# Performance work log

Hardware: AMD Instinct MI355X
Metric: run time of the kernel (lower is better)

Reference implementation:

```python
import jax, jax.numpy as jnp
import numpy as np

B, D, H, O = 32, 128, 256, 10


def setup_inputs() -> dict:
    key = jax.random.key(0)
    ks = jax.random.split(key, 8)
    return {
        "t": jax.random.uniform(ks[0], (1,), dtype=jnp.float32),
        "state_batch": jax.random.normal(ks[1], (2 * B, D), dtype=jnp.float32),
        "x0": jax.random.normal(ks[2], (B, D), dtype=jnp.float32),
        "x1": jax.random.normal(ks[3], (B, D), dtype=jnp.float32),
        "W1": jax.random.normal(ks[4], (D, H), dtype=jnp.float32) / np.sqrt(D),
        "b1": jax.random.normal(ks[5], (H,), dtype=jnp.float32) * 0.01,
        "W2": jax.random.normal(ks[6], (H, O), dtype=jnp.float32) / np.sqrt(H),
        "b2": jax.random.normal(ks[7], (O,), dtype=jnp.float32) * 0.01,
    }


def reference(t, state_batch, x0, x1, W1, b1, W2, b2):
    b = x0.shape[0]
    deviation, dev_velocity = state_batch[:b], state_batch[b:]  # [B,D] each
    tt = t[0]
    window = 4.0 * tt * (1.0 - tt)
    # point on the perturbed path
    x = x0 + tt * (x1 - x0) + window * deviation  # [B,D]

    def f_single(xs):  # [D] -> [O]
        return jnp.tanh(xs @ W1 + b1) @ W2 + b2

    def G_single(xs):  # [D] -> [D,D] pullback metric J^T J + eps I
        J = jax.jacrev(f_single)(xs)  # [O,D] (O small -> reverse mode)
        return J.T @ J + 1e-4 * jnp.eye(xs.shape[0], dtype=xs.dtype)

    # dG[b,i,j,k] = d G_ij / d x_k  -- replaces the torch double autograd loop
    dG = jax.vmap(jax.jacfwd(G_single))(x)  # [B,D,D,D]
    dG = dG / (jnp.sqrt(jnp.sum(dG * dG, axis=(1, 2, 3), keepdims=True)) + 1e-6)
    # Christoffel symbols (first kind, up to normalization as in source)
    Gamma = 0.5 * (dG + jnp.transpose(dG, (0, 2, 1, 3)) - jnp.transpose(dG, (0, 3, 1, 2)))
    a = -jnp.einsum('bijk,bj,bk->bi', Gamma, dev_velocity, dev_velocity)
    a = a / (jnp.linalg.norm(dev_velocity, axis=1, keepdims=True) + 1e-6)
    restoration = -0.1 * deviation
    return jnp.concatenate([dev_velocity, a + restoration], axis=0)  # [2B,D]
```

## Files before the change

### kernel.cpp

```cpp
#include <hip/hip_runtime.h>
#include <hip/hip_bf16.h>


#define NB 32

#define OP    0
#define OE    65536
#define OCW   163840
#define OAUN  245760
#define OVN   249856

template<int BF> __device__ __forceinline__ float ld(const void* p, int i) {
  if constexpr (BF) return __bfloat162float(((const __hip_bfloat16*)p)[i]);
  else return ((const float*)p)[i];
}
template<int BF> __device__ __forceinline__ void st(void* p, int i, float v) {
  if constexpr (BF) ((__hip_bfloat16*)p)[i] = __float2bfloat16(v);
  else ((float*)p)[i] = v;
}
__device__ __forceinline__ float b2f(unsigned short u) {
  return __uint_as_float(((unsigned int)u) << 16);
}
template<int BF> __device__ __forceinline__ float4 ld4(const void* p, int i) {
  if constexpr (BF) {
    ushort4 u = *(const ushort4*)((const unsigned short*)p + i);
    return make_float4(b2f(u.x), b2f(u.y), b2f(u.z), b2f(u.w));
  } else {
    return *(const float4*)((const float*)p + i);
  }
}

__device__ __forceinline__ int blocksniff(const void* sb, int* sh) {
  if (threadIdx.x == 0) *sh = 0;
  __syncthreads();
  float v = fabsf(__bfloat162float(((const __hip_bfloat16*)sb)[threadIdx.x & 255]));
  if (!(v < 1000.0f)) atomicOr(sh, 1);
  __syncthreads();
  return (*sh == 0) ? 1 : 0;
}

#define LXS   0
#define LVS   128
#define LW2   256
#define LYS   2816
#define LRED  2832
#define LF1   2880
#define LEL   4416
#define LSW2  7488
#define LCL   10560
#define LCL2  10660
#define LTOT  10760

#define F1ACC(wv, gidx) do { \
    const float* sp_ = &sm[LSW2 + (gidx)*12]; \
    float4 s0_ = *(const float4*)sp_; \
    float4 s1_ = *(const float4*)(sp_+4); \
    float2 s2_ = *(const float2*)(sp_+8); \
    fa[0]+=(wv)*s0_.x; fa[1]+=(wv)*s0_.y; fa[2]+=(wv)*s0_.z; fa[3]+=(wv)*s0_.w; \
    fa[4]+=(wv)*s1_.x; fa[5]+=(wv)*s1_.y; fa[6]+=(wv)*s1_.z; fa[7]+=(wv)*s1_.w; \
    fa[8]+=(wv)*s2_.x; fa[9]+=(wv)*s2_.y; \
  } while (0)

template<int BF>
__device__ void k1_body(const void* tin, const void* sbin, const void* x0in,
                        const void* x1in, const void* W1in, const void* b1in,
                        const void* W2in, float* ws, float* sm) {
  int bid = blockIdx.x, t = threadIdx.x;
  if (bid >= NB) {
    int row = bid - NB;
    float* colh = sm;
    if (t < 128) colh[t] = ld<BF>(W1in, t * 256 + row);
    __syncthreads();
    float pacc = 0.f;
    for (int d = 0; d < 128; d += 4) {
      float4 c4 = *(const float4*)&colh[d];
      pacc += c4.x * ld<BF>(W1in, (d + 0) * 256 + t);
      pacc += c4.y * ld<BF>(W1in, (d + 1) * 256 + t);
      pacc += c4.z * ld<BF>(W1in, (d + 2) * 256 + t);
      pacc += c4.w * ld<BF>(W1in, (d + 3) * 256 + t);
    }
    ws[OP + row * 256 + t] = pacc;
    return;
  }
  int b = bid;
  int w = t >> 6;
  float tt = ld<BF>(tin, 0);
  float window = 4.f * tt * (1.f - tt);
  if (t < 128) {
    float dev = ld<BF>(sbin, b * 128 + t);
    float v   = ld<BF>(sbin, (NB + b) * 128 + t);
    float x0v = ld<BF>(x0in, b * 128 + t);
    float x1v = ld<BF>(x1in, b * 128 + t);
    sm[LXS + t] = x0v + tt * (x1v - x0v) + window * dev;
    sm[LVS + t] = v;
  }
  for (int i = t; i < 2560; i += 256) sm[LW2 + i] = ld<BF>(W2in, i);
  __syncthreads();
  float hacc = ld<BF>(b1in, t), wacc = 0.f;
  for (int d = 0; d < 128; d += 4) {
    float4 xv = *(const float4*)&sm[LXS + d];
    float4 vv = *(const float4*)&sm[LVS + d];
    float w0 = ld<BF>(W1in, (d + 0) * 256 + t);
    float w1 = ld<BF>(W1in, (d + 1) * 256 + t);
    float w2 = ld<BF>(W1in, (d + 2) * 256 + t);
    float w3 = ld<BF>(W1in, (d + 3) * 256 + t);
    hacc += w0 * xv.x + w1 * xv.y + w2 * xv.z + w3 * xv.w;
    wacc += w0 * vv.x + w1 * vv.y + w2 * vv.z + w3 * vv.w;
  }
  float z  = tanhf(hacc);
  float sg = 1.f - z * z;
  float ug = -2.f * z * sg;
  float w2r[10];
  #pragma unroll
  for (int o = 0; o < 10; ++o) w2r[o] = sm[LW2 + t * 10 + o];
  #pragma unroll
  for (int o = 0; o < 10; ++o) sm[LSW2 + t * 12 + o] = sg * w2r[o];
  float cval = ug * wacc * wacc;
  float rv[11];
  #pragma unroll
  for (int o = 0; o < 10; ++o) rv[o] = cval * w2r[o];
  rv[10] = (t < 128) ? sm[LVS + t] * sm[LVS + t] : 0.f;
  #pragma unroll
  for (int o = 0; o < 11; ++o) {
    float v = rv[o];
    #pragma unroll
    for (int m = 32; m > 0; m >>= 1) v += __shfl_xor(v, m);
    if ((t & 63) == 0) sm[LRED + w * 12 + o] = v;
  }
  __syncthreads();
  if (t < 11) {
    float s = sm[LRED + t] + sm[LRED + 12 + t] + sm[LRED + 24 + t] + sm[LRED + 36 + t];
    if (t < 10) sm[LYS + t] = s;
    else        ws[OVN + b] = sqrtf(s);
  }
  int half = t >> 7, r = t & 127;
  float fa[10];
  #pragma unroll
  for (int o = 0; o < 10; ++o) fa[o] = 0.f;
  {
    const int gbase = half * 128;
    for (int gg = 0; gg < 128; gg += 4) {
      int g = gbase + gg;
      float4 w4 = ld4<BF>(W1in, r * 256 + g);
      F1ACC(w4.x, g + 0);
      F1ACC(w4.y, g + 1);
      F1ACC(w4.z, g + 2);
      F1ACC(w4.w, g + 3);
    }
  }
  if (half) {
    #pragma unroll
    for (int o = 0; o < 10; ++o) sm[LF1 + r * 12 + o] = fa[o];
  }
  __syncthreads();
  if (!half) {
    float aun = 0.f;
    #pragma unroll
    for (int o = 0; o < 10; ++o) {
      float f = fa[o] + sm[LF1 + r * 12 + o];
      sm[LF1 + r * 12 + o] = f;
      aun += f * sm[LYS + o];
    }
    ws[OAUN + b * 128 + t] = aun;
  }
  __syncthreads();
  float er[10];
  #pragma unroll
  for (int o = 0; o < 10; ++o) er[o] = 0.f;
  for (int d = 0; d < 128; ++d) {
    float w1v = ld<BF>(W1in, d * 256 + t);
    const float* fp = &sm[LF1 + d * 12];
    float4 a0 = *(const float4*)fp;
    float4 a1 = *(const float4*)(fp + 4);
    float2 a2 = *(const float2*)(fp + 8);
    er[0] += w1v * a0.x; er[1] += w1v * a0.y; er[2] += w1v * a0.z; er[3] += w1v * a0.w;
    er[4] += w1v * a1.x; er[5] += w1v * a1.y; er[6] += w1v * a1.z; er[7] += w1v * a1.w;
    er[8] += w1v * a2.x; er[9] += w1v * a2.y;
  }
  #pragma unroll
  for (int o = 0; o < 10; ++o) sm[LEL + t * 12 + o] = er[o];
  {
    float* gp = ws + OE + (b * 256 + t) * 12;
    *(float4*)gp       = make_float4(er[0], er[1], er[2], er[3]);
    *(float4*)(gp + 4) = make_float4(er[4], er[5], er[6], er[7]);
    *(float4*)(gp + 8) = make_float4(er[8], er[9], ug, 0.f);
  }
  __syncthreads();
  float cpart = 0.f;
  if (t < 200) {
    int gh = (t >= 100) ? 1 : 0;
    int idx = t - gh * 100;
    int o = idx / 10, p = idx - o * 10;
    const float* sa = &sm[LSW2 + gh * 1536 + o];
    const float* sb = &sm[LEL  + gh * 1536 + p];
    #pragma unroll 4
    for (int g = 0; g < 128; ++g) cpart += sa[g * 12] * sb[g * 12];
    if (gh) sm[LCL2 + idx] = cpart;
  }
  __syncthreads();
  if (t < 100) sm[LCL + t] = cpart + sm[LCL2 + t];
  __syncthreads();
  #pragma unroll
  for (int o = 0; o < 10; ++o) {
    float cw = 0.f;
    #pragma unroll
    for (int p = 0; p < 10; ++p) cw += sm[LCL + o * 10 + p] * w2r[p];
    ws[OCW + b * 2560 + o * 256 + t] = cw;
  }
}

__global__ __launch_bounds__(256) void K1(const void* tin, const void* sbin,
                                          const void* x0in, const void* x1in,
                                          const void* W1in, const void* b1in,
                                          const void* W2in, float* ws) {
  __shared__ int sh;
  __shared__ __align__(16) float sm[LTOT];
  int bf = blocksniff(sbin, &sh);
  if (bf) k1_body<1>(tin, sbin, x0in, x1in, W1in, b1in, W2in, ws, sm);
  else    k1_body<0>(tin, sbin, x0in, x1in, W1in, b1in, W2in, ws, sm);
}

template<int BF>
__device__ void k2_body(const void* sbin, const void* W2in, void* out, float* ws,
                        float* rec, float* w2h, float* red) {
  int b = blockIdx.x, t = threadIdx.x;
  int w = t >> 6;
  {
    float4* rec4 = (float4*)rec;
    const float4* src = (const float4*)(ws + OE + b * 3072);
    for (int i = t; i < 768; i += 256) rec4[i] = src[i];
  }
  for (int i = t; i < 3072; i += 256) {
    int r = i / 12, c = i - r * 12;
    w2h[i] = (c < 10) ? ld<BF>(W2in, r * 10 + c) : 0.f;
  }
  __syncthreads();
  float cwr[10], er[10], w2r[10];
  #pragma unroll
  for (int o = 0; o < 10; ++o) cwr[o] = ws[OCW + b * 2560 + o * 256 + t];
  float uT;
  {
    float4 e0 = *(const float4*)&rec[t * 12];
    float4 e1 = *(const float4*)&rec[t * 12 + 4];
    float4 e2 = *(const float4*)&rec[t * 12 + 8];
    er[0]=e0.x; er[1]=e0.y; er[2]=e0.z; er[3]=e0.w;
    er[4]=e1.x; er[5]=e1.y; er[6]=e1.z; er[7]=e1.w;
    er[8]=e2.x; er[9]=e2.y; uT = e2.z;
    float4 p0 = *(const float4*)&w2h[t * 12];
    float4 p1 = *(const float4*)&w2h[t * 12 + 4];
    float2 p2 = *(const float2*)&w2h[t * 12 + 8];
    w2r[0]=p0.x; w2r[1]=p0.y; w2r[2]=p0.z; w2r[3]=p0.w;
    w2r[4]=p1.x; w2r[5]=p1.y; w2r[6]=p1.z; w2r[7]=p1.w;
    w2r[8]=p2.x; w2r[9]=p2.y;
  }
  float acc = 0.f;
  for (int i0 = 0; i0 < 64; i0 += 8) {
    float ph[8];
    #pragma unroll
    for (int j = 0; j < 8; ++j)
      ph[j] = ws[OP + (w * 64 + i0 + j) * 256 + t];
    #pragma unroll
    for (int j = 0; j < 8; ++j) {
      int h = w * 64 + i0 + j;
      const float* rp = &rec[h * 12];
      float4 E0 = *(const float4*)rp;
      float4 E1 = *(const float4*)(rp + 4);
      float4 E2 = *(const float4*)(rp + 8);
      const float* wp = &w2h[h * 12];
      float4 W0 = *(const float4*)wp;
      float4 W1v = *(const float4*)(wp + 4);
      float4 W2v = *(const float4*)(wp + 8);
      float R = E0.x*w2r[0] + E0.y*w2r[1] + E0.z*w2r[2] + E0.w*w2r[3]
              + E1.x*w2r[4] + E1.y*w2r[5] + E1.z*w2r[6] + E1.w*w2r[7]
              + E2.x*w2r[8] + E2.y*w2r[9];
      float Rt = W0.x*er[0] + W0.y*er[1] + W0.z*er[2] + W0.w*er[3]
               + W1v.x*er[4] + W1v.y*er[5] + W1v.z*er[6] + W1v.w*er[7]
               + W2v.x*er[8] + W2v.y*er[9];
      float Qd = W0.x*cwr[0] + W0.y*cwr[1] + W0.z*cwr[2] + W0.w*cwr[3]
               + W1v.x*cwr[4] + W1v.y*cwr[5] + W1v.z*cwr[6] + W1v.w*cwr[7]
               + W2v.x*cwr[8] + W2v.y*cwr[9];
      acc += E2.z * ph[j] * (ph[j] * Qd + R * Rt);
    }
  }
  acc *= uT;
  #pragma unroll
  for (int m = 32; m > 0; m >>= 1) acc += __shfl_xor(acc, m);
  if ((t & 63) == 0) red[w] = acc;
  __syncthreads();
  float F = sqrtf(fmaxf(2.f * (red[0] + red[1] + red[2] + red[3]), 0.f));
  float denom = (F + 1e-6f) * (ws[OVN + b] + 1e-6f);
  if (t < 128) {
    st<BF>(out, b * 128 + t, ld<BF>(sbin, (NB + b) * 128 + t));
    float dev = ld<BF>(sbin, b * 128 + t);
    float val = -ws[OAUN + b * 128 + t] / denom - 0.1f * dev;
    st<BF>(out, (NB + b) * 128 + t, val);
  }
}

__global__ __launch_bounds__(256) void K2(const void* sbin, const void* W2in,
                                          void* out, float* ws) {
  __shared__ int sh;
  __shared__ __align__(16) float rec[3072];
  __shared__ __align__(16) float w2h[3072];
  __shared__ float red[4];
  int bf = blocksniff(sbin, &sh);
  if (bf) k2_body<1>(sbin, W2in, out, ws, rec, w2h, red);
  else    k2_body<0>(sbin, W2in, out, ws, rec, w2h, red);
}

extern "C" void kernel_launch(void* const* d_in, const int* in_sizes, int n_in,
                              void* d_out, int out_size, void* d_ws, size_t ws_size,
                              hipStream_t stream) {
  float* ws = (float*)d_ws;
  const void* tin  = d_in[0];
  const void* sbin = d_in[1];
  const void* x0in = d_in[2];
  const void* x1in = d_in[3];
  const void* W1in = d_in[4];
  const void* b1in = d_in[5];
  const void* W2in = d_in[6];

  K1<<<dim3(288), dim3(256), 0, stream>>>(tin, sbin, x0in, x1in, W1in, b1in, W2in, ws);
  K2<<<dim3(32),  dim3(256), 0, stream>>>(sbin, W2in, d_out, ws);
}
```

Baseline: 102.3 us.

## Fuse two kernels into one with device-scope flag sync on the P matrix

```diff
diff --git a/kernel.cpp b/kernel.cpp
--- a/kernel.cpp
+++ b/kernel.cpp
@@ -5,10 +5,9 @@
 #define NB 32
 
 #define OP    0
-#define OE    65536
-#define OCW   163840
-#define OAUN  245760
-#define OVN   249856
+
+__device__ int g_pdone = 0;
+__device__ int g_bdone = 0;
 
 template<int BF> __device__ __forceinline__ float ld(const void* p, int i) {
   if constexpr (BF) return __bfloat162float(((const __hip_bfloat16*)p)[i]);
@@ -21,12 +20,17 @@
 __device__ __forceinline__ float b2f(unsigned short u) {
   return __uint_as_float(((unsigned int)u) << 16);
 }
-template<int BF> __device__ __forceinline__ float4 ld4(const void* p, int i) {
+template<int BF> __device__ __forceinline__ void ld8v(const void* p, int i, float* o) {
   if constexpr (BF) {
-    ushort4 u = *(const ushort4*)((const unsigned short*)p + i);
-    return make_float4(b2f(u.x), b2f(u.y), b2f(u.z), b2f(u.w));
+    uint4 u = *(const uint4*)((const unsigned short*)p + i);
+    o[0] = b2f((unsigned short)(u.x & 0xffff)); o[1] = b2f((unsigned short)(u.x >> 16));
+    o[2] = b2f((unsigned short)(u.y & 0xffff)); o[3] = b2f((unsigned short)(u.y >> 16));
+    o[4] = b2f((unsigned short)(u.z & 0xffff)); o[5] = b2f((unsigned short)(u.z >> 16));
+    o[6] = b2f((unsigned short)(u.w & 0xffff)); o[7] = b2f((unsigned short)(u.w >> 16));
   } else {
-    return *(const float4*)((const float*)p + i);
+    float4 a = *(const float4*)((const float*)p + i);
+    float4 b = *(const float4*)((const float*)p + i + 4);
+    o[0]=a.x; o[1]=a.y; o[2]=a.z; o[3]=a.w; o[4]=b.x; o[5]=b.y; o[6]=b.z; o[7]=b.w;
   }
 }
 
@@ -49,7 +53,8 @@
 #define LSW2  7488
 #define LCL   10560
 #define LCL2  10660
-#define LTOT  10760
+#define LW2P  10760
+#define LTOT  13832
 
 #define F1ACC(wv, gidx) do { \
     const float* sp_ = &sm[LSW2 + (gidx)*12]; \
@@ -62,9 +67,9 @@
   } while (0)
 
 template<int BF>
-__device__ void k1_body(const void* tin, const void* sbin, const void* x0in,
+__device__ void fk_body(const void* tin, const void* sbin, const void* x0in,
                         const void* x1in, const void* W1in, const void* b1in,
-                        const void* W2in, float* ws, float* sm) {
+                        const void* W2in, void* out, float* ws, float* sm) {
   int bid = blockIdx.x, t = threadIdx.x;
   if (bid >= NB) {
     int row = bid - NB;
@@ -80,6 +85,11 @@
       pacc += c4.w * ld<BF>(W1in, (d + 3) * 256 + t);
     }
     ws[OP + row * 256 + t] = pacc;
+    __syncthreads();
+    if (t == 0) {
+      __threadfence();
+      __hip_atomic_fetch_add(&g_pdone, 1, __ATOMIC_RELEASE, __HIP_MEMORY_SCOPE_AGENT);
+    }
     return;
   }
   int b = bid;
@@ -115,6 +125,10 @@
   for (int o = 0; o < 10; ++o) w2r[o] = sm[LW2 + t * 10 + o];
   #pragma unroll
   for (int o = 0; o < 10; ++o) sm[LSW2 + t * 12 + o] = sg * w2r[o];
+  for (int i = t; i < 3072; i += 256) {
+    int r = i / 12, c = i - r * 12;
+    sm[LW2P + i] = (c < 10) ? sm[LW2 + r * 10 + c] : 0.f;
+  }
   float cval = ug * wacc * wacc;
   float rv[11];
   #pragma unroll
@@ -131,7 +145,7 @@
   if (t < 11) {
     float s = sm[LRED + t] + sm[LRED + 12 + t] + sm[LRED + 24 + t] + sm[LRED + 36 + t];
     if (t < 10) sm[LYS + t] = s;
-    else        ws[OVN + b] = sqrtf(s);
+    else        sm[LYS + 10] = sqrtf(s);
   }
   int half = t >> 7, r = t & 127;
   float fa[10];
@@ -139,13 +153,14 @@
   for (int o = 0; o < 10; ++o) fa[o] = 0.f;
   {
     const int gbase = half * 128;
-    for (int gg = 0; gg < 128; gg += 4) {
+    for (int gg = 0; gg < 128; gg += 8) {
       int g = gbase + gg;
-      float4 w4 = ld4<BF>(W1in, r * 256 + g);
-      F1ACC(w4.x, g + 0);
-      F1ACC(w4.y, g + 1);
-      F1ACC(w4.z, g + 2);
-      F1ACC(w4.w, g + 3);
+      float wv[8];
+      ld8v<BF>(W1in, r * 256 + g, wv);
+      F1ACC(wv[0], g + 0); F1ACC(wv[1], g + 1);
+      F1ACC(wv[2], g + 2); F1ACC(wv[3], g + 3);
+      F1ACC(wv[4], g + 4); F1ACC(wv[5], g + 5);
+      F1ACC(wv[6], g + 6); F1ACC(wv[7], g + 7);
     }
   }
   if (half) {
@@ -153,15 +168,14 @@
     for (int o = 0; o < 10; ++o) sm[LF1 + r * 12 + o] = fa[o];
   }
   __syncthreads();
+  float aun = 0.f;
   if (!half) {
-    float aun = 0.f;
     #pragma unroll
     for (int o = 0; o < 10; ++o) {
       float f = fa[o] + sm[LF1 + r * 12 + o];
       sm[LF1 + r * 12 + o] = f;
       aun += f * sm[LYS + o];
     }
-    ws[OAUN + b * 128 + t] = aun;
   }
   __syncthreads();
   float er[10];
@@ -179,12 +193,8 @@
   }
   #pragma unroll
   for (int o = 0; o < 10; ++o) sm[LEL + t * 12 + o] = er[o];
-  {
-    float* gp = ws + OE + (b * 256 + t) * 12;
-    *(float4*)gp       = make_float4(er[0], er[1], er[2], er[3]);
-    *(float4*)(gp + 4) = make_float4(er[4], er[5], er[6], er[7]);
-    *(float4*)(gp + 8) = make_float4(er[8], er[9], ug, 0.f);
-  }
+  sm[LEL + t * 12 + 10] = ug;
+  sm[LEL + t * 12 + 11] = 0.f;
   __syncthreads();
   float cpart = 0.f;
   if (t < 200) {
@@ -200,59 +210,20 @@
   __syncthreads();
   if (t < 100) sm[LCL + t] = cpart + sm[LCL2 + t];
   __syncthreads();
+  float cwr[10];
   #pragma unroll
   for (int o = 0; o < 10; ++o) {
     float cw = 0.f;
     #pragma unroll
     for (int p = 0; p < 10; ++p) cw += sm[LCL + o * 10 + p] * w2r[p];
-    ws[OCW + b * 2560 + o * 256 + t] = cw;
-  }
-}
-
-__global__ __launch_bounds__(256) void K1(const void* tin, const void* sbin,
-                                          const void* x0in, const void* x1in,
-                                          const void* W1in, const void* b1in,
-                                          const void* W2in, float* ws) {
-  __shared__ int sh;
-  __shared__ __align__(16) float sm[LTOT];
-  int bf = blocksniff(sbin, &sh);
-  if (bf) k1_body<1>(tin, sbin, x0in, x1in, W1in, b1in, W2in, ws, sm);
-  else    k1_body<0>(tin, sbin, x0in, x1in, W1in, b1in, W2in, ws, sm);
-}
-
-template<int BF>
-__device__ void k2_body(const void* sbin, const void* W2in, void* out, float* ws,
-                        float* rec, float* w2h, float* red) {
-  int b = blockIdx.x, t = threadIdx.x;
-  int w = t >> 6;
-  {
-    float4* rec4 = (float4*)rec;
-    const float4* src = (const float4*)(ws + OE + b * 3072);
-    for (int i = t; i < 768; i += 256) rec4[i] = src[i];
-  }
-  for (int i = t; i < 3072; i += 256) {
-    int r = i / 12, c = i - r * 12;
-    w2h[i] = (c < 10) ? ld<BF>(W2in, r * 10 + c) : 0.f;
-  }
-  __syncthreads();
-  float cwr[10], er[10], w2r[10];
-  #pragma unroll
-  for (int o = 0; o < 10; ++o) cwr[o] = ws[OCW + b * 2560 + o * 256 + t];
-  float uT;
-  {
-    float4 e0 = *(const float4*)&rec[t * 12];
-    float4 e1 = *(const float4*)&rec[t * 12 + 4];
-    float4 e2 = *(const float4*)&rec[t * 12 + 8];
-    er[0]=e0.x; er[1]=e0.y; er[2]=e0.z; er[3]=e0.w;
-    er[4]=e1.x; er[5]=e1.y; er[6]=e1.z; er[7]=e1.w;
-    er[8]=e2.x; er[9]=e2.y; uT = e2.z;
-    float4 p0 = *(const float4*)&w2h[t * 12];
-    float4 p1 = *(const float4*)&w2h[t * 12 + 4];
-    float2 p2 = *(const float2*)&w2h[t * 12 + 8];
-    w2r[0]=p0.x; w2r[1]=p0.y; w2r[2]=p0.z; w2r[3]=p0.w;
-    w2r[4]=p1.x; w2r[5]=p1.y; w2r[6]=p1.z; w2r[7]=p1.w;
-    w2r[8]=p2.x; w2r[9]=p2.y;
-  }
+    cwr[o] = cw;
+  }
+  if (t == 0) {
+    while (__hip_atomic_load(&g_pdone, __ATOMIC_ACQUIRE, __HIP_MEMORY_SCOPE_AGENT) < 256)
+      __builtin_amdgcn_s_sleep(2);
+  }
+  __syncthreads();
+  __threadfence();
   float acc = 0.f;
   for (int i0 = 0; i0 < 64; i0 += 8) {
     float ph[8];
@@ -262,11 +233,11 @@
     #pragma unroll
     for (int j = 0; j < 8; ++j) {
       int h = w * 64 + i0 + j;
-      const float* rp = &rec[h * 12];
+      const float* rp = &sm[LEL + h * 12];
       float4 E0 = *(const float4*)rp;
       float4 E1 = *(const float4*)(rp + 4);
       float4 E2 = *(const float4*)(rp + 8);
-      const float* wp = &w2h[h * 12];
+      const float* wp = &sm[LW2P + h * 12];
       float4 W0 = *(const float4*)wp;
       float4 W1v = *(const float4*)(wp + 4);
       float4 W2v = *(const float4*)(wp + 8);
@@ -282,30 +253,38 @@
       acc += E2.z * ph[j] * (ph[j] * Qd + R * Rt);
     }
   }
-  acc *= uT;
+  acc *= ug;
   #pragma unroll
   for (int m = 32; m > 0; m >>= 1) acc += __shfl_xor(acc, m);
-  if ((t & 63) == 0) red[w] = acc;
-  __syncthreads();
-  float F = sqrtf(fmaxf(2.f * (red[0] + red[1] + red[2] + red[3]), 0.f));
-  float denom = (F + 1e-6f) * (ws[OVN + b] + 1e-6f);
+  if ((t & 63) == 0) sm[LRED + w] = acc;
+  __syncthreads();
+  float F = sqrtf(fmaxf(2.f * (sm[LRED] + sm[LRED+1] + sm[LRED+2] + sm[LRED+3]), 0.f));
+  float denom = (F + 1e-6f) * (sm[LYS + 10] + 1e-6f);
   if (t < 128) {
     st<BF>(out, b * 128 + t, ld<BF>(sbin, (NB + b) * 128 + t));
     float dev = ld<BF>(sbin, b * 128 + t);
-    float val = -ws[OAUN + b * 128 + t] / denom - 0.1f * dev;
+    float val = -aun / denom - 0.1f * dev;
     st<BF>(out, (NB + b) * 128 + t, val);
   }
-}
-
-__global__ __launch_bounds__(256) void K2(const void* sbin, const void* W2in,
-                                          void* out, float* ws) {
+  __syncthreads();
+  if (t == 0) {
+    int old = __hip_atomic_fetch_add(&g_bdone, 1, __ATOMIC_ACQ_REL, __HIP_MEMORY_SCOPE_AGENT);
+    if (old == NB - 1) {
+      __hip_atomic_store(&g_pdone, 0, __ATOMIC_RELAXED, __HIP_MEMORY_SCOPE_AGENT);
+      __hip_atomic_store(&g_bdone, 0, __ATOMIC_RELAXED, __HIP_MEMORY_SCOPE_AGENT);
+    }
+  }
+}
+
+__global__ __launch_bounds__(256, 2) void FK(const void* tin, const void* sbin,
+                                             const void* x0in, const void* x1in,
+                                             const void* W1in, const void* b1in,
+                                             const void* W2in, void* out, float* ws) {
   __shared__ int sh;
-  __shared__ __align__(16) float rec[3072];
-  __shared__ __align__(16) float w2h[3072];
-  __shared__ float red[4];
+  __shared__ __align__(16) float sm[LTOT];
   int bf = blocksniff(sbin, &sh);
-  if (bf) k2_body<1>(sbin, W2in, out, ws, rec, w2h, red);
-  else    k2_body<0>(sbin, W2in, out, ws, rec, w2h, red);
+  if (bf) fk_body<1>(tin, sbin, x0in, x1in, W1in, b1in, W2in, out, ws, sm);
+  else    fk_body<0>(tin, sbin, x0in, x1in, W1in, b1in, W2in, out, ws, sm);
 }
 
 extern "C" void kernel_launch(void* const* d_in, const int* in_sizes, int n_in,
@@ -320,6 +299,5 @@
   const void* b1in = d_in[5];
   const void* W2in = d_in[6];
 
-  K1<<<dim3(288), dim3(256), 0, stream>>>(tin, sbin, x0in, x1in, W1in, b1in, W2in, ws);
-  K2<<<dim3(32),  dim3(256), 0, stream>>>(sbin, W2in, d_out, ws);
-}
+  FK<<<dim3(NB + 256), dim3(256), 0, stream>>>(tin, sbin, x0in, x1in, W1in, b1in, W2in, d_out, ws);
+}
```

Measured after the change: 106.1 us. 1.04x slower.
